# Kernel tuning notes

Measured on AMD Instinct MI355X. Metric: run time of the kernel, lower is better.

The kernel has to match this reference:

```python
import jax, jax.numpy as jnp
import numpy as np

N, E, F_IN, H, D = 50000, 800000, 128, 4, 32


def setup_inputs() -> dict:
    key = jax.random.key(0)
    k_x, k_e, k_w, k_al, k_ar = jax.random.split(key, 5)
    x = jax.random.normal(k_x, (N, F_IN), dtype=jnp.float32)
    edge_index = jax.random.randint(k_e, (2, E), 0, N, dtype=jnp.int32).astype(jnp.int64)
    # xavier-uniform-like scales
    s_w = float(np.sqrt(6.0 / (F_IN + H * D)))
    s_a = float(np.sqrt(6.0 / (D + 1)))
    W = jax.random.uniform(k_w, (F_IN, H * D), jnp.float32, -s_w, s_w)
    att_l = jax.random.uniform(k_al, (H, D), jnp.float32, -s_a, s_a)
    att_r = jax.random.uniform(k_ar, (H, D), jnp.float32, -s_a, s_a)
    bias = jnp.zeros((H * D,), jnp.float32)
    return {"x": x, "edge_index": edge_index, "W": W, "att_l": att_l, "att_r": att_r, "bias": bias}


def reference(x, edge_index, W, att_l, att_r, bias):
    num_nodes = x.shape[0]
    n_heads, head_dim = att_l.shape
    h = (x @ W).reshape(num_nodes, n_heads, head_dim)          # [N,H,D]
    alpha_l = jnp.einsum('nhd,hd->nh', h, att_l)               # [N,H]
    alpha_r = jnp.einsum('nhd,hd->nh', h, att_r)               # [N,H]
    from_idx, to_idx = edge_index[0], edge_index[1]
    att = alpha_l[from_idx] + alpha_r[to_idx]                  # [E,H]
    att = jax.nn.leaky_relu(att, negative_slope=0.2)
    # segment softmax over edges grouped by destination node (shift by global
    # per-head max, exactly as the source's _softmax effectively does)
    att = att - jax.lax.stop_gradient(jnp.max(att, axis=0, keepdims=True))
    ex = jnp.exp(att)                                          # [E,H]
    denom = jax.ops.segment_sum(ex, to_idx, num_segments=num_nodes)  # [N,H]
    att_n = ex / (denom[to_idx] + 1e-9)                        # [E,H]
    # scatter-weighted aggregation: out[n] = sum_{e: to=n} att[e] * h[from[e]]
    msgs = att_n[:, :, None] * h[from_idx]                     # [E,H,D]
    out = jax.ops.segment_sum(msgs, to_idx, num_segments=num_nodes)  # [N,H,D]
    out = out.reshape(num_nodes, n_heads * head_dim) + bias
    return out
```

## Files before the change

### kernel.cpp

```cpp
#include <hip/hip_runtime.h>
#include <cstdint>

#define N_NODES 50000
#define N_EDGES 800000
#define F_IN    128
#define N_HEADS 4
#define HEAD_DIM 32
#define F_OUT   128

#define NBUCK   391
#define NPB     128
#define KA_GRID 512
#define EPB     1563
#define CAPA    24
#define REC_CAP 2560
#define STAGE_CAP REC_CAP
#define NSTRIP  (N_NODES / 16)
#define NGEMM   ((NSTRIP + 3) / 4)

typedef unsigned int uint32;
typedef unsigned short ushort;
typedef __attribute__((ext_vector_type(8))) short short8v;
typedef __attribute__((ext_vector_type(4))) float float4v;

typedef __attribute__((address_space(1))) const ushort gushort;
typedef __attribute__((address_space(3))) ushort lushort;

__device__ __forceinline__ ushort f2bf(float f) {
    uint32 u = __float_as_uint(f);
    return (ushort)((u + 0x7FFFu + ((u >> 16) & 1u)) >> 16);
}


__device__ __forceinline__ int block_scan_excl_256(int v, int* p_total)
{
    const int t = threadIdx.x, lane = t & 63, wv = t >> 6;
    int incl = v;
#pragma unroll
    for (int d = 1; d < 64; d <<= 1) {
        int u = __shfl_up(incl, d);
        if (lane >= d) incl += u;
    }
    __shared__ int wsum[4];
    if (lane == 63) wsum[wv] = incl;
    __syncthreads();
    int woff = 0;
#pragma unroll
    for (int j = 0; j < 4; ++j) {
        int s = wsum[j];
        if (j < wv) woff += s;
    }
    if (p_total) *p_total = wsum[0] + wsum[1] + wsum[2] + wsum[3];
    __syncthreads();
    return woff + incl - v;
}

__global__ __launch_bounds__(256) void k_prep(const float* __restrict__ W,
    ushort* __restrict__ WTF)
{
    const int id = blockIdx.x * 256 + threadIdx.x;
    if (id >= 32 * 64) return;
    const int tile = id >> 6, l = id & 63;
    const int q = l >> 4, c15 = l & 15;
    const int nt = tile >> 2, kt = tile & 3;
    short8v hv, lv;
#pragma unroll
    for (int j = 0; j < 8; ++j) {
        const int k = kt * 32 + q * 8 + j;
        const float w = W[k * F_OUT + nt * 16 + c15];
        const ushort hi = f2bf(w);
        const float hif = __uint_as_float((uint32)hi << 16);
        hv[j] = (short)hi;
        lv[j] = (short)f2bf(w - hif);
    }
    *(short8v*)&WTF[tile * 512 + l * 8]         = hv;
    *(short8v*)&WTF[16384 + tile * 512 + l * 8] = lv;
}

__global__ __launch_bounds__(256, 2) void k_bin_gemm(
    const int* __restrict__ ei, const float* __restrict__ x,
    const ushort* __restrict__ WTF,
    const float* __restrict__ attl, const float* __restrict__ attr,
    uint32* __restrict__ priv, int* __restrict__ cnts,
    uint32* __restrict__ hbq, float* __restrict__ aLp, float* __restrict__ aRp)
{
    __shared__ __attribute__((aligned(16))) char lds_buf[65536];

    if (blockIdx.x < KA_GRID) {
        int* cur = (int*)lds_buf;
        const int sb = blockIdx.x, t = threadIdx.x;
        for (int bb = t; bb < NBUCK; bb += 256) cur[bb] = 0;
        __syncthreads();
        const int e0 = sb * EPB;
        const int lim = min(EPB, N_EDGES - e0);
        for (int i = t; i < lim; i += 256) {
            const int from = ei[e0 + i];
            const int to   = ei[N_EDGES + e0 + i];
            const int b = to >> 7;
            const int slot = atomicAdd(&cur[b], 1);
            if (slot < CAPA)
                priv[((size_t)b * KA_GRID + sb) * CAPA + slot] =
                    (uint32)from | ((uint32)(to & 127) << 16);
        }
        __syncthreads();
        for (int bb = t; bb < NBUCK; bb += 256)
            cnts[sb * NBUCK + bb] = min(cur[bb], CAPA);
        return;
    }

    const int bid   = blockIdx.x - KA_GRID;
    const int lane  = threadIdx.x & 63;
    const int wv    = threadIdx.x >> 6;
    const int q     = lane >> 4;
    const int c15   = lane & 15;

    ushort* wt = (ushort*)lds_buf;
#pragma unroll
    for (int i = 0; i < 16; ++i) {
        const int chunk = wv * 16 + i;
        __builtin_amdgcn_global_load_lds(
            (gushort*)(WTF + chunk * 512 + lane * 8),
            (lushort*)(wt + chunk * 512), 16, 0, 0);
    }
    __syncthreads();

    const int strip = bid * 4 + wv;
    if (strip >= NSTRIP) return;
    const int row0 = strip * 16;

    const float* xrow = x + (size_t)(row0 + c15) * F_IN + q * 8;
    short8v ahi[4], alo[4];
#pragma unroll
    for (int kt = 0; kt < 4; ++kt) {
        const float4 f0 = *(const float4*)(xrow + kt * 32);
        const float4 f1 = *(const float4*)(xrow + kt * 32 + 4);
        const float fs[8] = {f0.x, f0.y, f0.z, f0.w, f1.x, f1.y, f1.z, f1.w};
#pragma unroll
        for (int j = 0; j < 8; ++j) {
            const ushort hi = f2bf(fs[j]);
            const float hif = __uint_as_float((uint32)hi << 16);
            ahi[kt][j] = (short)hi;
            alo[kt][j] = (short)f2bf(fs[j] - hif);
        }
    }

    float4v acc[8];
#pragma unroll
    for (int nt = 0; nt < 8; ++nt) {
        float4v a = {0.f, 0.f, 0.f, 0.f};
#pragma unroll
        for (int kt = 0; kt < 4; ++kt) {
            const short8v bh = *(const short8v*)(wt + (nt * 4 + kt) * 512 + lane * 8);
            const short8v bl = *(const short8v*)(wt + 16384 + (nt * 4 + kt) * 512 + lane * 8);
            a = __builtin_amdgcn_mfma_f32_16x16x32_bf16(ahi[kt], bh, a, 0, 0, 0);
            a = __builtin_amdgcn_mfma_f32_16x16x32_bf16(alo[kt], bh, a, 0, 0, 0);
            a = __builtin_amdgcn_mfma_f32_16x16x32_bf16(ahi[kt], bl, a, 0, 0, 0);
        }
        acc[nt] = a;
    }

#pragma unroll
    for (int nt = 0; nt < 4; ++nt) {
#pragma unroll
        for (int r = 0; r < 4; ++r) {
            const uint32 d = (uint32)f2bf(acc[nt][r]) | ((uint32)f2bf(acc[nt + 4][r]) << 16);
            hbq[(size_t)(row0 + q * 4 + r) * 64 + nt * 16 + c15] = d;
        }
    }

    float aLacc[4][4] = {{0.f}}, aRacc[4][4] = {{0.f}};
#pragma unroll
    for (int nt = 0; nt < 8; ++nt) {
        const float alv = attl[nt * 16 + c15];
        const float arv = attr[nt * 16 + c15];
        const int hh = nt >> 1;
#pragma unroll
        for (int r = 0; r < 4; ++r) {
            aLacc[r][hh] = fmaf(acc[nt][r], alv, aLacc[r][hh]);
            aRacc[r][hh] = fmaf(acc[nt][r], arv, aRacc[r][hh]);
        }
    }
#pragma unroll
    for (int r = 0; r < 4; ++r) {
#pragma unroll
        for (int hh = 0; hh < 4; ++hh) {
            float vl = aLacc[r][hh], vr = aRacc[r][hh];
#pragma unroll
            for (int d = 1; d < 16; d <<= 1) {
                vl += __shfl_xor(vl, d);
                vr += __shfl_xor(vr, d);
            }
            if (c15 == hh) {
                const int row = row0 + q * 4 + r;
                const int pos = (hh & 1) * 2 + (hh >> 1);
                aLp[row * N_HEADS + pos] = vl;
                aRp[row * N_HEADS + pos] = vr;
            }
        }
    }
}

__global__ __launch_bounds__(256) void k_build(const uint32* __restrict__ priv,
    const int* __restrict__ cnts,
    int* __restrict__ count, int* __restrict__ offsets, int* __restrict__ rec_from)
{
    __shared__ uint32 stage[STAGE_CAP];
    __shared__ int so_s[KA_GRID];
    __shared__ ushort cts_s[KA_GRID];
    __shared__ int hist[NPB], curn[NPB];
    const int b = blockIdx.x, t = threadIdx.x;

    int c[2], s = 0;
#pragma unroll
    for (int j = 0; j < 2; ++j) {
        c[j] = cnts[(size_t)(2 * t + j) * NBUCK + b];
        s += c[j];
    }
    int total;
    int ex = block_scan_excl_256(s, &total);
#pragma unroll
    for (int j = 0; j < 2; ++j) {
        so_s[2 * t + j]  = ex;
        cts_s[2 * t + j] = (ushort)c[j];
        ex += c[j];
    }
    if (t < NPB) hist[t] = 0;
    __syncthreads();

    const uint32* pbase = priv + (size_t)b * KA_GRID * CAPA;
    for (int idx = t; idx < KA_GRID * CAPA; idx += 256) {
        const int sb = idx / CAPA;
        const int sl = idx - sb * CAPA;
        if (sl < (int)cts_s[sb]) {
            const int p = so_s[sb] + sl;
            if (p < STAGE_CAP) stage[p] = pbase[idx];
        }
    }
    __syncthreads();

    const int S = min(total, STAGE_CAP);
    for (int i = t; i < S; i += 256) atomicAdd(&hist[stage[i] >> 16], 1);
    __syncthreads();

    const int hv = (t < NPB) ? hist[t] : 0;
    int tot2;
    const int lo = block_scan_excl_256(hv, &tot2);
    const int rbase = b * REC_CAP;
    const int n = b * NPB + t;
    if (t < NPB && n < N_NODES) {
        count[n]   = hv;
        offsets[n] = rbase + lo;
    }
    if (t < NPB) curn[t] = lo;
    __syncthreads();

    for (int i = t; i < S; i += 256) {
        const uint32 e = stage[i];
        const int pos = atomicAdd(&curn[e >> 16], 1);
        rec_from[rbase + pos] = (int)(e & 0xFFFFu);
    }
}

__global__ __launch_bounds__(256) void k_agg(const int* __restrict__ rec_from,
    const int* __restrict__ count, const int* __restrict__ offsets,
    const float* __restrict__ aLp, const float* __restrict__ aRp,
    const uint32* __restrict__ hbq,
    const float* __restrict__ bias, float* __restrict__ out)
{
    const int lane = threadIdx.x & 63;
    const int n = blockIdx.x * 4 + (threadIdx.x >> 6);
    if (n >= N_NODES) return;
    const int cnt  = count[n];
    const int off  = offsets[n];
    const int hsel = (lane >> 5) * 2;
    const int l31  = lane & 31;
    const int gsel = lane & 32;
    const float2 arv = *(const float2*)&aRp[n * N_HEADS + hsel];
    float ax = 0.f, ay = 0.f, ds0 = 0.f, ds1 = 0.f;

    for (int base = 0; base < cnt; base += 32) {
        const int m = min(32, cnt - base);
        int vf = 0;
        float e0p = 0.f, e1p = 0.f;
        if (l31 < m) {
            vf = rec_from[off + base + l31];
            const float2 af = *(const float2*)&aLp[vf * N_HEADS + hsel];
            float t0 = af.x + arv.x; t0 = (t0 > 0.f) ? t0 : 0.2f * t0;
            float t1 = af.y + arv.y; t1 = (t1 > 0.f) ? t1 : 0.2f * t1;
            e0p = __expf(t0);
            e1p = __expf(t1);
        }
        int i = 0;
        for (; i + 8 <= m; i += 8) {
            int f[8]; uint32 h[8]; float e0[8], e1[8];
#pragma unroll
            for (int j = 0; j < 8; ++j) {
                const int s = gsel | (i + j);
                f[j]  = __shfl(vf, s);
                e0[j] = __shfl(e0p, s);
                e1[j] = __shfl(e1p, s);
            }
#pragma unroll
            for (int j = 0; j < 8; ++j) h[j] = hbq[(size_t)f[j] * 64 + lane];
#pragma unroll
            for (int j = 0; j < 8; ++j) {
                ax = fmaf(e0[j], __uint_as_float(h[j] << 16), ax);
                ay = fmaf(e1[j], __uint_as_float(h[j] & 0xFFFF0000u), ay);
                ds0 += e0[j]; ds1 += e1[j];
            }
        }
        for (; i + 4 <= m; i += 4) {
            int f[4]; uint32 h[4]; float e0[4], e1[4];
#pragma unroll
            for (int j = 0; j < 4; ++j) {
                const int s = gsel | (i + j);
                f[j]  = __shfl(vf, s);
                e0[j] = __shfl(e0p, s);
                e1[j] = __shfl(e1p, s);
            }
#pragma unroll
            for (int j = 0; j < 4; ++j) h[j] = hbq[(size_t)f[j] * 64 + lane];
#pragma unroll
            for (int j = 0; j < 4; ++j) {
                ax = fmaf(e0[j], __uint_as_float(h[j] << 16), ax);
                ay = fmaf(e1[j], __uint_as_float(h[j] & 0xFFFF0000u), ay);
                ds0 += e0[j]; ds1 += e1[j];
            }
        }
        for (; i < m; ++i) {
            const int s = gsel | i;
            const int f = __shfl(vf, s);
            const uint32 hv = hbq[(size_t)f * 64 + lane];
            const float e0 = __shfl(e0p, s), e1 = __shfl(e1p, s);
            ax = fmaf(e0, __uint_as_float(hv << 16), ax);
            ay = fmaf(e1, __uint_as_float(hv & 0xFFFF0000u), ay);
            ds0 += e0; ds1 += e1;
        }
    }
    const float inv0 = 1.0f / (ds0 + 1e-9f);
    const float inv1 = 1.0f / (ds1 + 1e-9f);
    out[n * F_OUT + lane]      = ax * inv0 + bias[lane];
    out[n * F_OUT + 64 + lane] = ay * inv1 + bias[64 + lane];
}

extern "C" void kernel_launch(void* const* d_in, const int* in_sizes, int n_in,
                              void* d_out, int out_size, void* d_ws, size_t ws_size,
                              hipStream_t stream)
{
    const float* x    = (const float*)d_in[0];
    const int*   ei   = (const int*)d_in[1];
    const float* W    = (const float*)d_in[2];
    const float* attl = (const float*)d_in[3];
    const float* attr = (const float*)d_in[4];
    const float* bias = (const float*)d_in[5];
    float* out = (float*)d_out;

    char* p = (char*)d_ws;
    auto carve = [&](size_t bytes) -> char* {
        char* q = p;
        p += (bytes + 255) & ~size_t(255);
        return q;
    };
    uint32* hbq      = (uint32*)carve((size_t)N_NODES * 64 * 4);
    uint32* priv     = (uint32*)carve((size_t)NBUCK * KA_GRID * CAPA * 4);
    int*    rec_from = (int*)carve((size_t)NBUCK * REC_CAP * 4);
    ushort* WTF      = (ushort*)carve(32768 * 2);
    float*  aLp      = (float*)carve((size_t)N_NODES * N_HEADS * 4);
    float*  aRp      = (float*)carve((size_t)N_NODES * N_HEADS * 4);
    int*    cnts     = (int*)carve((size_t)KA_GRID * NBUCK * 4);
    int*    count    = (int*)carve((size_t)N_NODES * 4);
    int*    offsets  = (int*)carve((size_t)N_NODES * 4);

    k_prep<<<8, 256, 0, stream>>>(W, WTF);
    k_bin_gemm<<<KA_GRID + NGEMM, 256, 0, stream>>>(ei, x, WTF,
                                                    attl, attr, priv, cnts,
                                                    hbq, aLp, aRp);
    k_build<<<NBUCK, 256, 0, stream>>>(priv, cnts, count, offsets, rec_from);
    k_agg<<<(N_NODES + 3) / 4, 256, 0, stream>>>(rec_from, count, offsets,
                                                 aLp, aRp, hbq, bias, out);
}
```

Before: 163.9 us.

## Replace fixed-capacity per-bucket slots with a compacted per-block bucket sort

The binning blocks now make two passes: they first build a bucket histogram, scan it into per-bucket offsets, and then scatter edge records into an LDS stage in bucket order. Each block writes its whole sorted chunk contiguously to global memory, along with per-bucket counts and offsets in bucket-major layout. The build kernel no longer scans the sparse 24-slot-per-block arrays. Each thread instead copies its blocks' contiguous runs, which removes the capacity truncation and the sparse strided reads. The cost is a second pass over the destination indices in the binning kernel, plus serial per-thread copy loops in the build kernel.

After: 154.0 us. 6.0% less time.

```diff
diff --git a/kernel.cpp b/kernel.cpp
--- a/kernel.cpp
+++ b/kernel.cpp
@@ -12,7 +12,7 @@
 #define NPB     128
 #define KA_GRID 512
 #define EPB     1563
-#define CAPA    24
+#define EPB_PAD 1568
 #define REC_CAP 2560
 #define STAGE_CAP REC_CAP
 #define NSTRIP  (N_NODES / 16)
@@ -81,30 +81,49 @@
     const int* __restrict__ ei, const float* __restrict__ x,
     const ushort* __restrict__ WTF,
     const float* __restrict__ attl, const float* __restrict__ attr,
-    uint32* __restrict__ priv, int* __restrict__ cnts,
+    uint32* __restrict__ blockarr, int* __restrict__ cnts, int* __restrict__ offs,
     uint32* __restrict__ hbq, float* __restrict__ aLp, float* __restrict__ aRp)
 {
     __shared__ __attribute__((aligned(16))) char lds_buf[65536];
 
     if (blockIdx.x < KA_GRID) {
-        int* cur = (int*)lds_buf;
+        int*    cur = (int*)lds_buf;
+        int*    off = cur + 512;
+        uint32* stg = (uint32*)(off + 512);
         const int sb = blockIdx.x, t = threadIdx.x;
-        for (int bb = t; bb < NBUCK; bb += 256) cur[bb] = 0;
-        __syncthreads();
+
+        cur[t] = 0; cur[t + 256] = 0;
+        __syncthreads();
+
         const int e0 = sb * EPB;
         const int lim = min(EPB, N_EDGES - e0);
+        for (int i = t; i < lim; i += 256)
+            atomicAdd(&cur[ei[N_EDGES + e0 + i] >> 7], 1);
+        __syncthreads();
+
+        const int c0 = cur[2 * t], c1 = cur[2 * t + 1];
+        const int ex = block_scan_excl_256(c0 + c1, nullptr);
+        off[2 * t]     = ex;
+        off[2 * t + 1] = ex + c0;
+        __syncthreads();
+
+        for (int bb = t; bb < NBUCK; bb += 256) {
+            cnts[(size_t)bb * KA_GRID + sb] = cur[bb];
+            offs[(size_t)bb * KA_GRID + sb] = off[bb];
+        }
+        __syncthreads();
+
         for (int i = t; i < lim; i += 256) {
             const int from = ei[e0 + i];
             const int to   = ei[N_EDGES + e0 + i];
-            const int b = to >> 7;
-            const int slot = atomicAdd(&cur[b], 1);
-            if (slot < CAPA)
-                priv[((size_t)b * KA_GRID + sb) * CAPA + slot] =
-                    (uint32)from | ((uint32)(to & 127) << 16);
-        }
-        __syncthreads();
-        for (int bb = t; bb < NBUCK; bb += 256)
-            cnts[sb * NBUCK + bb] = min(cur[bb], CAPA);
+            const int pos = atomicAdd(&off[to >> 7], 1);
+            stg[pos] = (uint32)from | ((uint32)(to & 127) << 16);
+        }
+        __syncthreads();
+
+        uint32* dst = blockarr + (size_t)sb * EPB_PAD;
+        for (int i = t; i < lim; i += 256)
+            dst[i] = stg[i];
         return;
     }
 
@@ -200,41 +219,34 @@
     }
 }
 
-__global__ __launch_bounds__(256) void k_build(const uint32* __restrict__ priv,
-    const int* __restrict__ cnts,
+__global__ __launch_bounds__(256) void k_build(const uint32* __restrict__ blockarr,
+    const int* __restrict__ cnts, const int* __restrict__ offs,
     int* __restrict__ count, int* __restrict__ offsets, int* __restrict__ rec_from)
 {
     __shared__ uint32 stage[STAGE_CAP];
-    __shared__ int so_s[KA_GRID];
-    __shared__ ushort cts_s[KA_GRID];
     __shared__ int hist[NPB], curn[NPB];
     const int b = blockIdx.x, t = threadIdx.x;
 
-    int c[2], s = 0;
+    int c[2], o[2];
 #pragma unroll
     for (int j = 0; j < 2; ++j) {
-        c[j] = cnts[(size_t)(2 * t + j) * NBUCK + b];
-        s += c[j];
+        c[j] = cnts[(size_t)b * KA_GRID + 2 * t + j];
+        o[j] = offs[(size_t)b * KA_GRID + 2 * t + j];
     }
     int total;
-    int ex = block_scan_excl_256(s, &total);
+    int ex = block_scan_excl_256(c[0] + c[1], &total);
+    if (t < NPB) hist[t] = 0;
+    __syncthreads();
+
 #pragma unroll
     for (int j = 0; j < 2; ++j) {
-        so_s[2 * t + j]  = ex;
-        cts_s[2 * t + j] = (ushort)c[j];
+        const int sb = 2 * t + j;
+        const uint32* src = blockarr + (size_t)sb * EPB_PAD + o[j];
+        for (int i = 0; i < c[j]; ++i) {
+            const int p = ex + i;
+            if (p < STAGE_CAP) stage[p] = src[i];
+        }
         ex += c[j];
-    }
-    if (t < NPB) hist[t] = 0;
-    __syncthreads();
-
-    const uint32* pbase = priv + (size_t)b * KA_GRID * CAPA;
-    for (int idx = t; idx < KA_GRID * CAPA; idx += 256) {
-        const int sb = idx / CAPA;
-        const int sl = idx - sb * CAPA;
-        if (sl < (int)cts_s[sb]) {
-            const int p = so_s[sb] + sl;
-            if (p < STAGE_CAP) stage[p] = pbase[idx];
-        }
     }
     __syncthreads();
 
@@ -362,20 +374,23 @@
         return q;
     };
     uint32* hbq      = (uint32*)carve((size_t)N_NODES * 64 * 4);
-    uint32* priv     = (uint32*)carve((size_t)NBUCK * KA_GRID * CAPA * 4);
+    uint32* blockarr = (uint32*)carve((size_t)KA_GRID * EPB_PAD * 4);
     int*    rec_from = (int*)carve((size_t)NBUCK * REC_CAP * 4);
     ushort* WTF      = (ushort*)carve(32768 * 2);
     float*  aLp      = (float*)carve((size_t)N_NODES * N_HEADS * 4);
     float*  aRp      = (float*)carve((size_t)N_NODES * N_HEADS * 4);
-    int*    cnts     = (int*)carve((size_t)KA_GRID * NBUCK * 4);
+    int*    cnts     = (int*)carve((size_t)NBUCK * KA_GRID * 4);
+    int*    offs     = (int*)carve((size_t)NBUCK * KA_GRID * 4);
     int*    count    = (int*)carve((size_t)N_NODES * 4);
     int*    offsets  = (int*)carve((size_t)N_NODES * 4);
 
     k_prep<<<8, 256, 0, stream>>>(W, WTF);
     k_bin_gemm<<<KA_GRID + NGEMM, 256, 0, stream>>>(ei, x, WTF,
-                                                    attl, attr, priv, cnts,
+                                                    attl, attr, blockarr,
+                                                    cnts, offs,
                                                     hbq, aLp, aRp);
-    k_build<<<NBUCK, 256, 0, stream>>>(priv, cnts, count, offsets, rec_from);
+    k_build<<<NBUCK, 256, 0, stream>>>(blockarr, cnts, offs,
+                                       count, offsets, rec_from);
     k_agg<<<(N_NODES + 3) / 4, 256, 0, stream>>>(rec_from, count, offsets,
                                                  aLp, aRp, hbq, bias, out);
 }
```
